# Performance work log

Hardware: AMD Instinct MI355X
Metric: run time of the kernel (lower is better)

## Reference

```python
import jax, jax.numpy as jnp
import numpy as np

NB_HEAD = 16
SIZE_PER_HEAD = 64


def setup_inputs() -> dict:
    key = jax.random.key(0)
    k1, k2 = jax.random.split(key)
    x = jax.random.normal(k1, (2, 2048, 1024), dtype=jnp.float32)
    kernel = jax.random.normal(k2, (3, 1024, NB_HEAD * SIZE_PER_HEAD), dtype=jnp.float32) * 0.02
    return {"x": x, "kernel": kernel}


def reference(x, kernel):
    B, S, D = x.shape
    H, dh = NB_HEAD, SIZE_PER_HEAD
    # QKV projections: [B,S,D] @ [D, H*dh] -> [B,S,H,dh] -> [B,H,S,dh]
    def proj(w):
        return jnp.einsum('bsd,de->bse', x, w).reshape(B, S, H, dh).transpose(0, 2, 1, 3)
    Q = proj(kernel[0])
    Ks = proj(kernel[1])
    V = proj(kernel[2])
    scores = jnp.einsum('bhqd,bhkd->bhqk', Q, Ks) / jnp.sqrt(jnp.float32(dh))
    attn = jax.nn.softmax(scores, axis=-1)
    z = jnp.einsum('bhqk,bhkd->bhqd', attn, V)  # [B,H,S,dh]
    return z.transpose(0, 2, 1, 3).reshape(B, S, H * dh)
```

## Files before the change

### kernel.cpp

```cpp
#include <hip/hip_runtime.h>
#include <hip/hip_bf16.h>

#define HB 16
#define DH 64
#define SQ 2048
#define BB 2

using f32x4 = __attribute__((ext_vector_type(4))) float;
using f32x16 = __attribute__((ext_vector_type(16))) float;
using s16x8 = __attribute__((ext_vector_type(8))) short;

__device__ __forceinline__ unsigned bfr(float f) {
    union { float f; unsigned u; } v; v.f = f;
    return (v.u + 0x7fffu + ((v.u >> 16) & 1u)) >> 16;
}
__device__ __forceinline__ unsigned pk2(float a, float b) { return bfr(a) | (bfr(b) << 16); }
__device__ __forceinline__ short f2bf(float f) { return (short)bfr(f); }

__device__ __forceinline__ int swz64(int r, int c) {
    return r * 64 + ((((c >> 3) ^ (r & 7)) & 7) << 3) + (c & 7);
}
__device__ __forceinline__ int swz32(int r, int c) {
    return r * 32 + ((((c >> 3) ^ ((r >> 1) & 3)) & 3) << 3) + (c & 7);
}

__device__ __forceinline__ void gll16(const short* g, short* l) {
    __builtin_amdgcn_global_load_lds(
        (const __attribute__((address_space(1))) unsigned int*)(uintptr_t)g,
        (__attribute__((address_space(3))) unsigned int*)(uintptr_t)l, 16, 0, 0);
}

__global__ __launch_bounds__(256) void cvt_x(const float* __restrict__ x, short* __restrict__ xb) {
    int i = (blockIdx.x * 256 + threadIdx.x) * 8;
    float4 v0 = *(const float4*)&x[i];
    float4 v1 = *(const float4*)&x[i + 4];
    uint4 u;
    u.x = pk2(v0.x, v0.y); u.y = pk2(v0.z, v0.w);
    u.z = pk2(v1.x, v1.y); u.w = pk2(v1.z, v1.w);
    *(uint4*)&xb[i] = u;
}

__device__ __forceinline__ int swzT(int n, int k) {
    return n * 64 + ((((k >> 3) ^ ((n >> 2) & 7)) & 7) << 3) + (k & 7);
}
__global__ __launch_bounds__(256) void cvt_wt(const float* __restrict__ w, short* __restrict__ wt) {
    __shared__ short T[64 * 64];
    int bid = blockIdx.x;
    int nt = bid & 15, kt = (bid >> 4) & 15, p = bid >> 8;
    const float* wp = w + p * 1048576 + (kt * 64) * 1024 + nt * 64;
    short* wtp = wt + p * 1048576 + (nt * 64) * 1024 + kt * 64;
    int t = threadIdx.x;
#pragma unroll
    for (int ps = 0; ps < 4; ps++) {
        int idx = ps * 1024 + t * 4;
        int r = idx >> 6, c = idx & 63;
        float4 v = *(const float4*)&wp[r * 1024 + c];
        T[swzT(c + 0, r)] = f2bf(v.x);
        T[swzT(c + 1, r)] = f2bf(v.y);
        T[swzT(c + 2, r)] = f2bf(v.z);
        T[swzT(c + 3, r)] = f2bf(v.w);
    }
    __syncthreads();
#pragma unroll
    for (int ps = 0; ps < 2; ps++) {
        int idx = ps * 2048 + t * 8;
        int n = idx >> 6, kc = idx & 63;
        s16x8 vv = *(const s16x8*)&T[swzT(n, kc)];
        *(s16x8*)&wtp[n * 1024 + kc] = vv;
    }
}

__global__ __launch_bounds__(256) void qkv_gemm(
    const short* __restrict__ xb, const short* __restrict__ wt, short* __restrict__ ws)
{
    __shared__ short Xs[2][128 * 32];
    __shared__ short Ns[2][128 * 32];
    const int tid = threadIdx.x;
    const int wv = tid >> 6, ln = tid & 63;
    const int bid = blockIdx.x;
    const int swz = (bid & 7) * 96 + (bid >> 3);
    const int mIdx = swz & 31, nIdx = swz >> 5;
    const int m0 = mIdx * 128;
    const int p = nIdx >> 3;
    const int n0 = (nIdx & 7) * 128;
    const short* wtp = wt + p * 1048576;

    const int wm = (wv & 1) * 64, wn = (wv >> 1) * 64;
    const int lr = ln & 15, lk = (ln >> 4) * 8;
    const int srow = ln >> 2;
    const int csw = (((ln & 3) ^ ((ln >> 3) & 3)) & 3) * 8;

    f32x4 acc[4][4] = {};

#define GSTAGE(k0_, bf_) do {                                                   \
        _Pragma("unroll")                                                       \
        for (int q = 0; q < 2; q++) {                                           \
            int call = wv * 2 + q;                                              \
            gll16(&xb[(m0 + call * 16 + srow) * 1024 + (k0_) + csw], &Xs[bf_][call * 512]); \
            gll16(&wtp[(n0 + call * 16 + srow) * 1024 + (k0_) + csw], &Ns[bf_][call * 512]); \
        }                                                                       \
    } while (0)

#define GCOMP(bf_) do {                                                         \
        s16x8 af[4], bg[4];                                                     \
        _Pragma("unroll")                                                       \
        for (int i = 0; i < 4; i++)                                             \
            af[i] = *(const s16x8*)&Xs[bf_][swz32(wm + i * 16 + lr, lk)];       \
        _Pragma("unroll")                                                       \
        for (int j = 0; j < 4; j++)                                             \
            bg[j] = *(const s16x8*)&Ns[bf_][swz32(wn + j * 16 + lr, lk)];       \
        __builtin_amdgcn_s_setprio(1);                                          \
        _Pragma("unroll")                                                       \
        for (int i = 0; i < 4; i++)                                             \
            _Pragma("unroll")                                                   \
            for (int j = 0; j < 4; j++)                                         \
                acc[i][j] = __builtin_amdgcn_mfma_f32_16x16x32_bf16(af[i], bg[j], acc[i][j], 0, 0, 0); \
        __builtin_amdgcn_s_setprio(0);                                          \
    } while (0)

    GSTAGE(0, 0);
    __syncthreads();
    for (int t = 0; t < 32; t++) {
        int cur = t & 1;
        if (t < 31) GSTAGE((t + 1) * 32, cur ^ 1);
        GCOMP(cur);
        __syncthreads();
    }

    short* qws = ws;
    short* kws = ws + BB * HB * SQ * DH;
    short* vtw = ws + 2 * BB * HB * SQ * DH;
#pragma unroll
    for (int i = 0; i < 4; i++) {
#pragma unroll
        for (int r = 0; r < 4; r++) {
            int row = m0 + wm + i * 16 + (ln >> 4) * 4 + r;
            int b = row >> 11, s = row & 2047;
#pragma unroll
            for (int j = 0; j < 4; j++) {
                int gcol = n0 + wn + j * 16 + (ln & 15);
                int h = gcol >> 6, dhi = gcol & 63;
                float v = acc[i][j][r];
                if (p == 0)      qws[((b * HB + h) * SQ + s) * DH + dhi] = f2bf(v * 0.1803368801f);
                else if (p == 1) kws[((b * HB + h) * SQ + s) * DH + dhi] = f2bf(v);
                else             vtw[((b * HB + h) * DH + dhi) * SQ + s] = f2bf(v);
            }
        }
    }
#undef GSTAGE
#undef GCOMP
}

__global__ __launch_bounds__(512, 4) void attn(
    const short* __restrict__ qws, const short* __restrict__ kws,
    const short* __restrict__ vtw, float* __restrict__ out)
{
    __shared__ __align__(16) short smem[32768];
    __shared__ float Lx[4][32];
    const int tid = threadIdx.x, wv = tid >> 6, ln = tid & 63;
    const int ws_ = wv & 3, g = wv >> 2;
    const int bid = blockIdx.x;
    const int swz = (bid & 7) * 64 + (bid >> 3);
    const int qt = swz & 15, bh = swz >> 4;
    const short* Q = qws + bh * SQ * DH;
    const short* K = kws + bh * SQ * DH;
    const short* VT = vtw + bh * DH * SQ;
    const int lq = ln & 31, lg = ln >> 5;
    const int q0w = qt * 128 + ws_ * 32;
    const int kvbase = g * 1024;

    const int csw = ((ln & 7) ^ ((ln >> 3) & 7)) * 8;
    const int klo = (ln >> 3) * DH + csw;
    const int vlo = (ln >> 3) * SQ + csw;

    s16x8 qf[4];
#pragma unroll
    for (int ks = 0; ks < 4; ks++)
        qf[ks] = *(const s16x8*)&Q[(q0w + lq) * DH + ks * 16 + lg * 8];

    f32x16 o0 = {}, o1 = {};
    float l = 0.f;

#define STAGE(t, bf_) do {                                          \
        short* Kd = smem + g * 16384 + (bf_) * 8192;                \
        short* Vd = Kd + 4096;                                      \
        const short* Kt = K + (kvbase + (t) * 64) * DH;             \
        const short* Vt = VT + kvbase + (t) * 64;                   \
        _Pragma("unroll")                                           \
        for (int jj = 0; jj < 2; jj++) {                            \
            int run = ws_ * 2 + jj;                                 \
            gll16(Kt + run * 8 * DH + klo, Kd + run * 512);         \
            gll16(Vt + run * 8 * SQ + vlo, Vd + run * 512);         \
        }                                                           \
    } while (0)

#define COMPUTE(bf_) do {                                                      \
        const short* Kr = smem + g * 16384 + (bf_) * 8192;                     \
        const short* Vr = Kr + 4096;                                           \
        f32x16 s0 = {}, s1 = {};                                               \
        __builtin_amdgcn_s_setprio(1);                                         \
        _Pragma("unroll")                                                      \
        for (int ks = 0; ks < 4; ks++) {                                       \
            s16x8 ka0 = *(const s16x8*)&Kr[swz64(lq, ks * 16 + lg * 8)];       \
            s16x8 ka1 = *(const s16x8*)&Kr[swz64(32 + lq, ks * 16 + lg * 8)];  \
            s0 = __builtin_amdgcn_mfma_f32_32x32x16_bf16(ka0, qf[ks], s0, 0, 0, 0); \
            s1 = __builtin_amdgcn_mfma_f32_32x32x16_bf16(ka1, qf[ks], s1, 0, 0, 0); \
        }                                                                      \
        __builtin_amdgcn_s_setprio(0);                                         \
        float p[32];                                                           \
        _Pragma("unroll")                                                      \
        for (int i = 0; i < 16; i++) p[i] = __builtin_amdgcn_exp2f(s0[i]);     \
        _Pragma("unroll")                                                      \
        for (int i = 0; i < 16; i++) p[16 + i] = __builtin_amdgcn_exp2f(s1[i]); \
        float a0 = 0.f, a1 = 0.f, a2 = 0.f, a3 = 0.f;                          \
        _Pragma("unroll")                                                      \
        for (int i = 0; i < 32; i += 4) {                                      \
            a0 += p[i]; a1 += p[i + 1]; a2 += p[i + 2]; a3 += p[i + 3];        \
        }                                                                      \
        l += (a0 + a1) + (a2 + a3);                                            \
        unsigned u[16];                                                        \
        _Pragma("unroll")                                                      \
        for (int qd = 0; qd < 8; qd++) {                                       \
            asm("v_cvt_pk_bf16_f32 %0, %1, %2" : "=v"(u[qd * 2]) : "v"(p[qd * 4 + 0]), "v"(p[qd * 4 + 1])); \
            asm("v_cvt_pk_bf16_f32 %0, %1, %2" : "=v"(u[qd * 2 + 1]) : "v"(p[qd * 4 + 2]), "v"(p[qd * 4 + 3])); \
        }                                                                      \
        _Pragma("unroll")                                                      \
        for (int a = 0; a < 2; a++)                                            \
            _Pragma("unroll")                                                  \
            for (int m2 = 0; m2 < 2; m2++)                                     \
                _Pragma("unroll")                                              \
                for (int j = 0; j < 2; j++)                                    \
                    asm("v_permlane32_swap_b32 %0, %1"                         \
                        : "+v"(u[(a * 4 + 2 * m2) * 2 + j]), "+v"(u[(a * 4 + 2 * m2 + 1) * 2 + j])); \
        __builtin_amdgcn_s_setprio(1);                                         \
        _Pragma("unroll")                                                      \
        for (int ks = 0; ks < 4; ks++) {                                       \
            int a = ks >> 1, m2 = ks & 1;                                      \
            union { unsigned w[4]; s16x8 v; } pa;                              \
            pa.w[0] = u[(a * 4 + 2 * m2) * 2];                                 \
            pa.w[1] = u[(a * 4 + 2 * m2) * 2 + 1];                             \
            pa.w[2] = u[(a * 4 + 2 * m2 + 1) * 2];                             \
            pa.w[3] = u[(a * 4 + 2 * m2 + 1) * 2 + 1];                         \
            s16x8 vb0 = *(const s16x8*)&Vr[swz64(lq, ks * 16 + lg * 8)];       \
            s16x8 vb1 = *(const s16x8*)&Vr[swz64(32 + lq, ks * 16 + lg * 8)];  \
            o0 = __builtin_amdgcn_mfma_f32_32x32x16_bf16(pa.v, vb0, o0, 0, 0, 0); \
            o1 = __builtin_amdgcn_mfma_f32_32x32x16_bf16(pa.v, vb1, o1, 0, 0, 0); \
        }                                                                      \
        __builtin_amdgcn_s_setprio(0);                                         \
    } while (0)

    STAGE(0, 0);
    __syncthreads();
    for (int t = 0; t < 16; t++) {
        int cur = t & 1;
        if (t < 15) STAGE(t + 1, cur ^ 1);
        COMPUTE(cur);
        __syncthreads();
    }

    float lt = l + __shfl_xor(l, 32);
    float* Lf = (float*)smem;
    if (g == 1) {
#pragma unroll
        for (int r = 0; r < 16; r++) {
            Lf[ws_ * 1024 + r * 64 + ln] = o0[r];
            Lf[8192 + ws_ * 1024 + r * 64 + ln] = o1[r];
        }
        if (lg == 0) Lx[ws_][lq] = lt;
    }
    __syncthreads();
    if (g == 0) {
        float inv = 1.0f / (lt + Lx[ws_][lq]);
        const int b = bh >> 4, h = bh & 15;
#pragma unroll
        for (int r = 0; r < 16; r++) {
            int qrow = (r & 3) + 8 * (r >> 2) + 4 * lg;
            float iv = __shfl(inv, qrow);
            float* op = out + ((long)(b * SQ + q0w + qrow)) * 1024 + h * 64 + lq;
            op[0]  = (o0[r] + Lf[ws_ * 1024 + r * 64 + ln]) * iv;
            op[32] = (o1[r] + Lf[8192 + ws_ * 1024 + r * 64 + ln]) * iv;
        }
    }
#undef STAGE
#undef COMPUTE
}

extern "C" void kernel_launch(void* const* d_in, const int* in_sizes, int n_in,
                              void* d_out, int out_size, void* d_ws, size_t ws_size,
                              hipStream_t stream) {
    const float* x = (const float*)d_in[0];
    const float* w = (const float*)d_in[1];
    short* ws = (short*)d_ws;
    short* xbf = (short*)d_out;
    short* wtb = (short*)d_out + 4194304;
    cvt_x<<<2048, 256, 0, stream>>>(x, xbf);
    cvt_wt<<<768, 256, 0, stream>>>(w, wtb);
    qkv_gemm<<<768, 256, 0, stream>>>(xbf, wtb, ws);
    attn<<<512, 512, 0, stream>>>(ws, ws + BB * HB * SQ * DH,
                                  ws + 2 * BB * HB * SQ * DH, (float*)d_out);
}
```

Measured before the change: 106.0 us.

## Fuse fp32-to-bf16 conversion of x into the QKV GEMM load stage

Removes the separate cvt_x kernel and has the QKV GEMM load fp32 x directly into registers. It converts with v_cvt_pk_bf16_f32 and writes the swizzled bf16 tile to LDS after the MFMA compute, overlapping the global loads with the compute. This drops one launch and the bf16 round trip of x through memory. In exchange, each GEMM block reads twice as many bytes of x, and x is re-read by all 24 N-tiles, which adds register pressure and load traffic inside the GEMM. Rounding also changes from the hand-written round-to-nearest-even to the hardware conversion instruction.

```diff
diff --git a/kernel.cpp b/kernel.cpp
--- a/kernel.cpp
+++ b/kernel.cpp
@@ -14,7 +14,6 @@
     union { float f; unsigned u; } v; v.f = f;
     return (v.u + 0x7fffu + ((v.u >> 16) & 1u)) >> 16;
 }
-__device__ __forceinline__ unsigned pk2(float a, float b) { return bfr(a) | (bfr(b) << 16); }
 __device__ __forceinline__ short f2bf(float f) { return (short)bfr(f); }
 
 __device__ __forceinline__ int swz64(int r, int c) {
@@ -28,16 +27,6 @@
     __builtin_amdgcn_global_load_lds(
         (const __attribute__((address_space(1))) unsigned int*)(uintptr_t)g,
         (__attribute__((address_space(3))) unsigned int*)(uintptr_t)l, 16, 0, 0);
-}
-
-__global__ __launch_bounds__(256) void cvt_x(const float* __restrict__ x, short* __restrict__ xb) {
-    int i = (blockIdx.x * 256 + threadIdx.x) * 8;
-    float4 v0 = *(const float4*)&x[i];
-    float4 v1 = *(const float4*)&x[i + 4];
-    uint4 u;
-    u.x = pk2(v0.x, v0.y); u.y = pk2(v0.z, v0.w);
-    u.z = pk2(v1.x, v1.y); u.w = pk2(v1.z, v1.w);
-    *(uint4*)&xb[i] = u;
 }
 
 __device__ __forceinline__ int swzT(int n, int k) {
@@ -71,7 +60,7 @@
 }
 
 __global__ __launch_bounds__(256) void qkv_gemm(
-    const short* __restrict__ xb, const short* __restrict__ wt, short* __restrict__ ws)
+    const float* __restrict__ x, const short* __restrict__ wt, short* __restrict__ ws)
 {
     __shared__ short Xs[2][128 * 32];
     __shared__ short Ns[2][128 * 32];
@@ -89,16 +78,36 @@
     const int lr = ln & 15, lk = (ln >> 4) * 8;
     const int srow = ln >> 2;
     const int csw = (((ln & 3) ^ ((ln >> 3) & 3)) & 3) * 8;
+    const int xr = tid >> 1;
+    const int xkh = (tid & 1) * 16;
+    const int xsw = (xr >> 1) & 3;
+    const int c0 = (tid & 1) * 2;
+    const int a0 = xr * 32 + ((c0 ^ xsw) & 3) * 8;
+    const int a1 = xr * 32 + (((c0 + 1) ^ xsw) & 3) * 8;
+    const float* xrow = &x[(m0 + xr) * 1024 + xkh];
 
     f32x4 acc[4][4] = {};
 
-#define GSTAGE(k0_, bf_) do {                                                   \
+#define WSTAGE(k0_, bf_) do {                                                   \
         _Pragma("unroll")                                                       \
         for (int q = 0; q < 2; q++) {                                           \
             int call = wv * 2 + q;                                              \
-            gll16(&xb[(m0 + call * 16 + srow) * 1024 + (k0_) + csw], &Xs[bf_][call * 512]); \
             gll16(&wtp[(n0 + call * 16 + srow) * 1024 + (k0_) + csw], &Ns[bf_][call * 512]); \
         }                                                                       \
+    } while (0)
+
+#define XWRITE(bf_) do {                                                        \
+        unsigned u0, u1, u2, u3, u4, u5, u6, u7;                                \
+        asm("v_cvt_pk_bf16_f32 %0, %1, %2" : "=v"(u0) : "v"(xv0.x), "v"(xv0.y)); \
+        asm("v_cvt_pk_bf16_f32 %0, %1, %2" : "=v"(u1) : "v"(xv0.z), "v"(xv0.w)); \
+        asm("v_cvt_pk_bf16_f32 %0, %1, %2" : "=v"(u2) : "v"(xv1.x), "v"(xv1.y)); \
+        asm("v_cvt_pk_bf16_f32 %0, %1, %2" : "=v"(u3) : "v"(xv1.z), "v"(xv1.w)); \
+        asm("v_cvt_pk_bf16_f32 %0, %1, %2" : "=v"(u4) : "v"(xv2.x), "v"(xv2.y)); \
+        asm("v_cvt_pk_bf16_f32 %0, %1, %2" : "=v"(u5) : "v"(xv2.z), "v"(xv2.w)); \
+        asm("v_cvt_pk_bf16_f32 %0, %1, %2" : "=v"(u6) : "v"(xv3.x), "v"(xv3.y)); \
+        asm("v_cvt_pk_bf16_f32 %0, %1, %2" : "=v"(u7) : "v"(xv3.z), "v"(xv3.w)); \
+        *(uint4*)&Xs[bf_][a0] = make_uint4(u0, u1, u2, u3);                     \
+        *(uint4*)&Xs[bf_][a1] = make_uint4(u4, u5, u6, u7);                     \
     } while (0)
 
 #define GCOMP(bf_) do {                                                         \
@@ -118,12 +127,28 @@
         __builtin_amdgcn_s_setprio(0);                                          \
     } while (0)
 
-    GSTAGE(0, 0);
+    {
+        float4 xv0 = *(const float4*)(xrow + 0);
+        float4 xv1 = *(const float4*)(xrow + 4);
+        float4 xv2 = *(const float4*)(xrow + 8);
+        float4 xv3 = *(const float4*)(xrow + 12);
+        WSTAGE(0, 0);
+        XWRITE(0);
+    }
     __syncthreads();
     for (int t = 0; t < 32; t++) {
-        int cur = t & 1;
-        if (t < 31) GSTAGE((t + 1) * 32, cur ^ 1);
+        int cur = t & 1, nb = cur ^ 1;
+        float4 xv0, xv1, xv2, xv3;
+        if (t < 31) {
+            const float* xs = xrow + (t + 1) * 32;
+            xv0 = *(const float4*)(xs + 0);
+            xv1 = *(const float4*)(xs + 4);
+            xv2 = *(const float4*)(xs + 8);
+            xv3 = *(const float4*)(xs + 12);
+            WSTAGE((t + 1) * 32, nb);
+        }
         GCOMP(cur);
+        if (t < 31) XWRITE(nb);
         __syncthreads();
     }
 
@@ -147,7 +172,8 @@
             }
         }
     }
-#undef GSTAGE
+#undef WSTAGE
+#undef XWRITE
 #undef GCOMP
 }
 
@@ -291,11 +317,9 @@
     const float* x = (const float*)d_in[0];
     const float* w = (const float*)d_in[1];
     short* ws = (short*)d_ws;
-    short* xbf = (short*)d_out;
-    short* wtb = (short*)d_out + 4194304;
-    cvt_x<<<2048, 256, 0, stream>>>(x, xbf);
+    short* wtb = (short*)d_out;
     cvt_wt<<<768, 256, 0, stream>>>(w, wtb);
-    qkv_gemm<<<768, 256, 0, stream>>>(xbf, wtb, ws);
+    qkv_gemm<<<768, 256, 0, stream>>>(x, wtb, ws);
     attn<<<512, 512, 0, stream>>>(ws, ws + BB * HB * SQ * DH,
                                   ws + 2 * BB * HB * SQ * DH, (float*)d_out);
 }
```

New measurement: 114.7 us. 1.08x slower.
